# Kernel tuning notes

Measured on AMD Instinct MI355X. Metric: run time of the kernel, lower is better.

The kernel has to match this reference:

```python
import jax, jax.numpy as jnp
import numpy as np

EPS = 1e-10
TOP_K = 2  # experts_per_token


def setup_inputs() -> dict:
    key = jax.random.key(0)
    k1, k2 = jax.random.split(key)
    dim, E = 2048, 64
    B, S = 4, 4096
    x = jax.random.normal(k1, (B * S, dim), dtype=jnp.float32)
    W = jax.random.normal(k2, (dim, E), dtype=jnp.float32) * (1.0 / np.sqrt(dim))
    b = jnp.zeros((E,), dtype=jnp.float32)
    return {"x": x, "W": W, "b": b, "batch_size": B, "seq_len": S}


def reference(x, W, b, batch_size, seq_len):
    E = W.shape[1]
    N = x.shape[0]  # batch_size * seq_len
    # gate + softmax + clamp
    scores = jax.nn.softmax(x @ W + b, axis=1)
    scores = jnp.clip(scores, EPS, 1.0 - EPS)
    # log-odds transform and rz loss over (seq, experts) per batch
    logits = jnp.log(scores / (1.0 - scores)).reshape(batch_size, seq_len, E)
    rz_loss = jnp.mean(jax.scipy.special.logsumexp(logits, axis=(1, 2)))
    # top-k experts per token
    top_scores, sel_idx = jax.lax.top_k(scores, TOP_K)  # (N, K) each
    flat_idx = sel_idx.reshape(-1)  # (N*K,)
    # histogram of assignments per expert (torch.histc with unit bins)
    num_tokens_per_expert = jax.ops.segment_sum(
        jnp.ones_like(flat_idx, dtype=jnp.float32), flat_idx, num_segments=E)
    # stable argsort groups slots by expert id, preserving token order
    perm = jnp.argsort(flat_idx, stable=True)  # (N*K,)
    top_scores_sorted = top_scores.reshape(-1)[perm]
    token_indices_experts_sorted = perm // TOP_K
    return (top_scores_sorted, token_indices_experts_sorted,
            num_tokens_per_expert, rz_loss)
```

## Files before the change

kernel.cpp:

```cpp
#include <hip/hip_runtime.h>
#include <math.h>

#define EPS_ 1e-10f
#define MARGIN 4e-3f

typedef __attribute__((ext_vector_type(8))) short sh8;
typedef __attribute__((ext_vector_type(4))) float fx4;

__device__ __forceinline__ bool betterf(float v, int i, float w, int j) {
    return (v > w) || (v == w && i < j);
}
__device__ __forceinline__ bool betterd(double v, int i, double w, int j) {
    return (v > w) || (v == w && i < j);
}
__device__ __forceinline__ unsigned short f2bf(float f) {
    unsigned u = __float_as_uint(f);
    u += 0x7fffu + ((u >> 16) & 1u);
    return (unsigned short)(u >> 16);
}
__device__ __forceinline__ float bf2f(unsigned short h) {
    return __uint_as_float(((unsigned)h) << 16);
}
__device__ __forceinline__ void cvt8(const float4 a, const float4 c, sh8& hi, sh8& lo) {
    const float v[8] = {a.x, a.y, a.z, a.w, c.x, c.y, c.z, c.w};
#pragma unroll
    for (int j = 0; j < 8; ++j) {
        const unsigned short h = f2bf(v[j]);
        hi[j] = (short)h;
        lo[j] = (short)f2bf(v[j] - bf2f(h));
    }
}

__global__ __launch_bounds__(256)
void wconv(const float* __restrict__ W, unsigned short* __restrict__ wf)
{
    const int gid = blockIdx.x * 256 + threadIdx.x;
    const int e = gid & 63, k = gid >> 6;
    const int s = k >> 5, kk = k & 31, bq = kk >> 3, j = kk & 7;
    const int t = e >> 4, n = e & 15;
    const int l = n + 16 * bq;
    const float w = W[(size_t)k * 64 + e];
    const unsigned short hi = f2bf(w);
    const unsigned short lo = f2bf(w - bf2f(hi));
    const size_t base = ((size_t)s * 4 + t) * 2;
    wf[(base + 0) * 512 + l * 8 + j] = hi;
    wf[(base + 1) * 512 + l * 8 + j] = lo;
}

#define NKS 4
__global__ __launch_bounds__(256, 4)
void gemm_mfma(const float* __restrict__ x, const unsigned short* __restrict__ wfg,
               const float* __restrict__ b, int dim, int N,
               float* __restrict__ ts, int* __restrict__ sel,
               float* __restrict__ rzrow,
               int* __restrict__ nflags, int* __restrict__ flaglist)
{
    __shared__ float red[3][64][17];

    const int tid  = threadIdx.x;
    const int lane = tid & 63;
    const int wv   = tid >> 6;
    const int r0   = blockIdx.x * 16;
    const int kslice = dim / NKS;
    const int k0   = wv * kslice;
    const int nstep = kslice / 32;

    const int m = lane & 15;
    const int q = lane >> 4;

    fx4 acc[4] = {};

    const float* xp = x + (size_t)(r0 + m) * dim + k0 + q * 8;
    const unsigned short* wbase = wfg + ((size_t)(k0 / 32) * 4096) + lane * 8;

    float4 xa = *(const float4*)xp;
    float4 xb = *(const float4*)(xp + 4);

    for (int w = 0; w < nstep; ++w) {
        sh8 ahi, alo;
        cvt8(xa, xb, ahi, alo);

        if (w + 1 < nstep) {
            xa = *(const float4*)(xp + (size_t)(w + 1) * 32);
            xb = *(const float4*)(xp + (size_t)(w + 1) * 32 + 4);
        }

        const unsigned short* wk = wbase + (size_t)w * 4096;
        sh8 bhi[4], blo[4];
#pragma unroll
        for (int t = 0; t < 4; ++t) {
            bhi[t] = __builtin_bit_cast(sh8, *(const int4*)(wk + (t * 2 + 0) * 512));
            blo[t] = __builtin_bit_cast(sh8, *(const int4*)(wk + (t * 2 + 1) * 512));
        }
#pragma unroll
        for (int t = 0; t < 4; ++t)
            acc[t] = __builtin_amdgcn_mfma_f32_16x16x32_bf16(ahi, bhi[t], acc[t], 0, 0, 0);
#pragma unroll
        for (int t = 0; t < 4; ++t)
            acc[t] = __builtin_amdgcn_mfma_f32_16x16x32_bf16(ahi, blo[t], acc[t], 0, 0, 0);
#pragma unroll
        for (int t = 0; t < 4; ++t)
            acc[t] = __builtin_amdgcn_mfma_f32_16x16x32_bf16(alo, bhi[t], acc[t], 0, 0, 0);
    }

    if (wv > 0) {
#pragma unroll
        for (int t = 0; t < 4; ++t)
#pragma unroll
            for (int i = 0; i < 4; ++i)
                red[wv - 1][lane][t * 4 + i] = acc[t][i];
    }
    __syncthreads();
    if (wv != 0) return;

#pragma unroll
    for (int s = 0; s < 3; ++s)
#pragma unroll
        for (int t = 0; t < 4; ++t)
#pragma unroll
            for (int i = 0; i < 4; ++i)
                acc[t][i] += red[s][lane][t * 4 + i];

    const int n = lane & 15;
    const int g = lane >> 4;
    float bb[4];
#pragma unroll
    for (int t = 0; t < 4; ++t) bb[t] = b[t * 16 + n];

#pragma unroll
    for (int i = 0; i < 4; ++i) {
        const int row = r0 + g * 4 + i;
        float z[4];
#pragma unroll
        for (int t = 0; t < 4; ++t) z[t] = acc[t][i] + bb[t];

        float v1 = -3.4e38f, v2 = -3.4e38f;
        int i1 = 1 << 30, i2 = 1 << 30;
#pragma unroll
        for (int t = 0; t < 4; ++t) {
            const float v = z[t];
            const int e = t * 16 + n;
            if (v > v1)      { v2 = v1; i2 = i1; v1 = v; i1 = e; }
            else if (v > v2) { v2 = v;  i2 = e; }
        }
#pragma unroll
        for (int mm = 1; mm < 16; mm <<= 1) {
            const float w1 = __shfl_xor(v1, mm, 16); const int j1 = __shfl_xor(i1, mm, 16);
            const float w2 = __shfl_xor(v2, mm, 16); const int j2 = __shfl_xor(i2, mm, 16);
            if (betterf(w1, j1, v1, i1)) {
                float nv2; int ni2;
                if (betterf(v1, i1, w2, j2)) { nv2 = v1; ni2 = i1; }
                else                         { nv2 = w2; ni2 = j2; }
                v1 = w1; i1 = j1; v2 = nv2; i2 = ni2;
            } else if (betterf(w1, j1, v2, i2)) { v2 = w1; i2 = j1; }
        }

        float m3 = -3.4e38f;
#pragma unroll
        for (int t = 0; t < 4; ++t) {
            const int e = t * 16 + n;
            const bool skip = (e == i1) || (e == i2);
            m3 = skip ? m3 : fmaxf(m3, z[t]);
        }
#pragma unroll
        for (int mm = 1; mm < 16; mm <<= 1) m3 = fmaxf(m3, __shfl_xor(m3, mm, 16));

        float sloc[4], ssum = 0.0f;
#pragma unroll
        for (int t = 0; t < 4; ++t) { sloc[t] = expf(z[t] - v1); ssum += sloc[t]; }
#pragma unroll
        for (int mm = 1; mm < 16; mm <<= 1) ssum += __shfl_xor(ssum, mm, 16);
        const float inv = 1.0f / ssum;
        float srz = 0.0f;
#pragma unroll
        for (int t = 0; t < 4; ++t) {
            float sc = fminf(fmaxf(sloc[t] * inv, EPS_), 1.0f - EPS_);
            srz += sc / (1.0f - sc);
        }
#pragma unroll
        for (int mm = 1; mm < 16; mm <<= 1) srz += __shfl_xor(srz, mm, 16);

        if (n == 0) {
            const float s1 = fminf(fmaxf(inv, EPS_), 1.0f - EPS_);
            const float s2 = fminf(fmaxf(expf(v2 - v1) * inv, EPS_), 1.0f - EPS_);
            ts[row * 2 + 0] = s1;
            ts[row * 2 + 1] = s2;
            sel[row * 2 + 0] = i1;
            sel[row * 2 + 1] = i2;
            rzrow[row] = srz;
            if ((v1 - v2) < MARGIN || (v2 - m3) < MARGIN) {
                const int slot = atomicAdd(nflags, 1);
                flaglist[slot] = row;
            }
        }
    }
}

__global__ __launch_bounds__(1024)
void fixup(const float* __restrict__ x, const float* __restrict__ W,
           const float* __restrict__ b, int dim,
           const int* __restrict__ nflags, const int* __restrict__ flaglist,
           float* __restrict__ ts, int* __restrict__ sel)
{
    __shared__ double red[1024];
    const int tid = threadIdx.x;
    const int e = tid & 63;
    const int q = tid >> 6;
    const int nf = *nflags;
    const int slice = dim >> 4;

    for (int f = blockIdx.x; f < nf; f += gridDim.x) {
        const int row = flaglist[f];
        const float* xr = x + (size_t)row * dim;
        const int k0 = q * slice;
        double a0 = 0.0, a1 = 0.0, a2 = 0.0, a3 = 0.0;
        for (int k = k0; k < k0 + slice; k += 4) {
            a0 = fma((double)xr[k + 0], (double)W[(size_t)(k + 0) * 64 + e], a0);
            a1 = fma((double)xr[k + 1], (double)W[(size_t)(k + 1) * 64 + e], a1);
            a2 = fma((double)xr[k + 2], (double)W[(size_t)(k + 2) * 64 + e], a2);
            a3 = fma((double)xr[k + 3], (double)W[(size_t)(k + 3) * 64 + e], a3);
        }
        red[tid] = (a0 + a1) + (a2 + a3);
        __syncthreads();
        for (int st = 512; st >= 64; st >>= 1) {
            if (tid < st) red[tid] += red[tid + st];
            __syncthreads();
        }
        if (tid < 64) {
            const double z = red[tid] + (double)b[e];
            double v1 = z, v2 = -1e300;
            int i1 = e, i2 = 1 << 30;
#pragma unroll
            for (int mm = 1; mm < 64; mm <<= 1) {
                const double w1 = __shfl_xor(v1, mm, 64); const int j1 = __shfl_xor(i1, mm, 64);
                const double w2 = __shfl_xor(v2, mm, 64); const int j2 = __shfl_xor(i2, mm, 64);
                if (betterd(w1, j1, v1, i1)) {
                    double nv2; int ni2;
                    if (betterd(v1, i1, w2, j2)) { nv2 = v1; ni2 = i1; }
                    else                         { nv2 = w2; ni2 = j2; }
                    v1 = w1; i1 = j1; v2 = nv2; i2 = ni2;
                } else if (betterd(w1, j1, v2, i2)) { v2 = w1; i2 = j1; }
            }
            float sl = expf((float)(z - v1));
            float ssum = sl;
#pragma unroll
            for (int mm = 1; mm < 64; mm <<= 1) ssum += __shfl_xor(ssum, mm, 64);
            const float inv = 1.0f / ssum;
            if (e == 0) {
                const float s1 = fminf(fmaxf(inv, EPS_), 1.0f - EPS_);
                const float s2 = fminf(fmaxf(expf((float)(v2 - v1)) * inv, EPS_), 1.0f - EPS_);
                ts[row * 2 + 0] = s1;
                ts[row * 2 + 1] = s2;
                sel[row * 2 + 0] = i1;
                sel[row * 2 + 1] = i2;
            }
        }
        __syncthreads();
    }
}

__global__ void hist_chunks(const int* __restrict__ sel, int nchunks,
                            int* __restrict__ hist, int* __restrict__ cnt2)
{
    __shared__ int cnt[64];
    const int lane = threadIdx.x;
    const int c = blockIdx.x;
    cnt[lane] = 0;
    __syncthreads();
    const int ex = sel[c * 64 + lane];
    atomicAdd(&cnt[ex], 1);
    __syncthreads();
    cnt2[(size_t)lane * nchunks + c] = cnt[lane];
    if (cnt[lane]) atomicAdd(&hist[lane], cnt[lane]);
}

__global__ void rz_batch(const float* __restrict__ rzrow,
                         const int* __restrict__ bs_p, const int* __restrict__ sl_p,
                         double* __restrict__ bsum)
{
    __shared__ double red[256];
    const int nb = bs_p[0];
    const int seq = sl_p[0];
    for (int bb = blockIdx.x; bb < nb; bb += gridDim.x) {
        double s = 0.0;
        for (int i = threadIdx.x; i < seq; i += 256)
            s += (double)rzrow[(size_t)bb * seq + i];
        red[threadIdx.x] = s;
        __syncthreads();
        for (int st = 128; st > 0; st >>= 1) {
            if (threadIdx.x < st) red[threadIdx.x] += red[threadIdx.x + st];
            __syncthreads();
        }
        if (threadIdx.x == 0) bsum[bb] = red[0];
        __syncthreads();
    }
}

__global__ void combine(const int* __restrict__ hist,
                        int* __restrict__ estart,
                        const double* __restrict__ bsum,
                        const int* __restrict__ bs_p,
                        float* __restrict__ out_cnt, float* __restrict__ out_rz)
{
    const int e = threadIdx.x;
    const int c0 = hist[e];
    int incl = c0;
#pragma unroll
    for (int mm = 1; mm < 64; mm <<= 1) {
        const int w = __shfl_up(incl, mm, 64);
        if (e >= mm) incl += w;
    }
    estart[e] = incl - c0;
    out_cnt[e] = (float)c0;
    if (e == 0) {
        const int nb = bs_p[0];
        double a = 0.0;
        for (int i = 0; i < nb; ++i) a += log(bsum[i]);
        out_rz[0] = (float)(a / nb);
    }
}

__global__ __launch_bounds__(1024)
void chunk_scan(const int* __restrict__ cnt2, const int* __restrict__ estart,
                int nchunks, int* __restrict__ cbase)
{
    __shared__ int sc[1024];
    const int e = blockIdx.x;
    const int t = threadIdx.x;
    const int v = (t < nchunks) ? cnt2[(size_t)e * nchunks + t] : 0;
    sc[t] = v;
    __syncthreads();
#pragma unroll
    for (int off = 1; off < 1024; off <<= 1) {
        const int add = (t >= off) ? sc[t - off] : 0;
        __syncthreads();
        sc[t] += add;
        __syncthreads();
    }
    if (t < nchunks)
        cbase[(size_t)t * 64 + e] = estart[e] + sc[t] - v;
}

__global__ void scatter(const int* __restrict__ sel, const float* __restrict__ ts,
                        const int* __restrict__ cbase,
                        float* __restrict__ out_sc, float* __restrict__ out_idx)
{
    __shared__ int shx[64];
    const int lane = threadIdx.x;
    const int c = blockIdx.x;
    const int idx = c * 64 + lane;
    const int ex = sel[idx];
    shx[lane] = ex;
    __syncthreads();
    int pre = 0;
#pragma unroll
    for (int j = 0; j < 64; ++j) pre += (int)((j < lane) && (shx[j] == ex));
    const int pos = cbase[c * 64 + ex] + pre;
    out_sc[pos]  = ts[idx];
    out_idx[pos] = (float)(idx >> 1);
}

extern "C" void kernel_launch(void* const* d_in, const int* in_sizes, int n_in,
                              void* d_out, int out_size, void* d_ws, size_t ws_size,
                              hipStream_t stream)
{
    const float* x = (const float*)d_in[0];
    const float* W = (const float*)d_in[1];
    const float* b = (const float*)d_in[2];
    const int* bs_p = (const int*)d_in[3];
    const int* sl_p = (const int*)d_in[4];

    const int E   = in_sizes[2];
    const int dim = in_sizes[1] / E;
    const int N   = in_sizes[0] / dim;
    const int total = N * 2;
    const int nchunks = total / 64;

    char* ws = (char*)d_ws;
    size_t off = 0;
    int*    hist     = (int*)(ws + off); off += 256;
    double* bsum     = (double*)(ws + off); off += 512;
    int*    nflags   = (int*)(ws + off); off += 256;
    int*    estart   = (int*)(ws + off); off += 256;
    float*  ts       = (float*)(ws + off); off += (size_t)total * 4;
    int*    sel      = (int*)(ws + off); off += (size_t)total * 4;
    int*    flaglist = (int*)(ws + off); off += (size_t)N * 4;
    float*  rzrow    = (float*)(ws + off); off += (size_t)N * 4;
    int*    cnt2     = (int*)(ws + off); off += (size_t)nchunks * 64 * 4;
    int*    cbase    = (int*)(ws + off); off += (size_t)nchunks * 64 * 4;
    unsigned short* wfg = (unsigned short*)(ws + off); off += (size_t)dim * 64 * 2 * 2;

    float* out_sc  = (float*)d_out;
    float* out_idx = out_sc + total;
    float* out_cnt = out_idx + total;
    float* out_rz  = out_cnt + E;

    hipMemsetAsync(ws, 0, 1280, stream);

    hipLaunchKernelGGL(wconv, dim3(dim * 64 / 256), dim3(256), 0, stream, W, wfg);
    hipLaunchKernelGGL(gemm_mfma, dim3(N / 16), dim3(256), 0, stream,
                       x, wfg, b, dim, N, ts, sel, rzrow, nflags, flaglist);
    hipLaunchKernelGGL(fixup, dim3(512), dim3(1024), 0, stream,
                       x, W, b, dim, nflags, flaglist, ts, sel);
    hipLaunchKernelGGL(hist_chunks, dim3(nchunks), dim3(64), 0, stream,
                       sel, nchunks, hist, cnt2);
    hipLaunchKernelGGL(rz_batch, dim3(64), dim3(256), 0, stream,
                       rzrow, bs_p, sl_p, bsum);
    hipLaunchKernelGGL(combine, dim3(1), dim3(64), 0, stream,
                       hist, estart, bsum, bs_p, out_cnt, out_rz);
    hipLaunchKernelGGL(chunk_scan, dim3(64), dim3(1024), 0, stream,
                       cnt2, estart, nchunks, cbase);
    hipLaunchKernelGGL(scatter, dim3(nchunks), dim3(64), 0, stream,
                       sel, ts, cbase, out_sc, out_idx);
}
```

Before: 102.4 us.

## Tile gate GEMM over 64 rows with 8 k-split waves and tree reduction

The gate GEMM block now handles 64 rows instead of 16 and splits K across 8 waves instead of 4. Each B fragment loaded from global memory is reused across four row tiles, with double-buffered weight loads. Partial sums are combined through a shared-memory tree reduction, and the softmax/top-2 epilogue is spread across all waves, one expert per lane. This cuts redundant weight traffic and per-row overhead, at the cost of far more accumulator registers (64 floats per lane), a larger shared-memory footprint, and more barriers.

```diff
diff --git a/kernel.cpp b/kernel.cpp
--- a/kernel.cpp
+++ b/kernel.cpp
@@ -47,140 +47,219 @@
     wf[(base + 1) * 512 + l * 8 + j] = lo;
 }
 
-#define NKS 4
-__global__ __launch_bounds__(256, 4)
+__global__ __launch_bounds__(512, 2)
 void gemm_mfma(const float* __restrict__ x, const unsigned short* __restrict__ wfg,
                const float* __restrict__ b, int dim, int N,
                float* __restrict__ ts, int* __restrict__ sel,
                float* __restrict__ rzrow,
                int* __restrict__ nflags, int* __restrict__ flaglist)
 {
-    __shared__ float red[3][64][17];
+    __shared__ float slots[4][64][65];
 
     const int tid  = threadIdx.x;
     const int lane = tid & 63;
     const int wv   = tid >> 6;
-    const int r0   = blockIdx.x * 16;
-    const int kslice = dim / NKS;
+    const int r0   = blockIdx.x * 64;
+    const int kslice = dim >> 3;
     const int k0   = wv * kslice;
-    const int nstep = kslice / 32;
+    const int nstep = kslice >> 5;
 
     const int m = lane & 15;
     const int q = lane >> 4;
 
-    fx4 acc[4] = {};
-
-    const float* xp = x + (size_t)(r0 + m) * dim + k0 + q * 8;
-    const unsigned short* wbase = wfg + ((size_t)(k0 / 32) * 4096) + lane * 8;
-
-    float4 xa = *(const float4*)xp;
-    float4 xb = *(const float4*)(xp + 4);
-
-    for (int w = 0; w < nstep; ++w) {
-        sh8 ahi, alo;
-        cvt8(xa, xb, ahi, alo);
-
-        if (w + 1 < nstep) {
-            xa = *(const float4*)(xp + (size_t)(w + 1) * 32);
-            xb = *(const float4*)(xp + (size_t)(w + 1) * 32 + 4);
-        }
-
-        const unsigned short* wk = wbase + (size_t)w * 4096;
-        sh8 bhi[4], blo[4];
-#pragma unroll
-        for (int t = 0; t < 4; ++t) {
-            bhi[t] = __builtin_bit_cast(sh8, *(const int4*)(wk + (t * 2 + 0) * 512));
-            blo[t] = __builtin_bit_cast(sh8, *(const int4*)(wk + (t * 2 + 1) * 512));
-        }
+    fx4 acc[4][4];
+#pragma unroll
+    for (int t = 0; t < 4; ++t)
+#pragma unroll
+        for (int te = 0; te < 4; ++te)
+            acc[t][te] = (fx4){0.f, 0.f, 0.f, 0.f};
+
+    const float* xp0 = x + (size_t)(r0 +  0 + m) * dim + k0 + q * 8;
+    const float* xp1 = x + (size_t)(r0 + 16 + m) * dim + k0 + q * 8;
+    const float* xp2 = x + (size_t)(r0 + 32 + m) * dim + k0 + q * 8;
+    const float* xp3 = x + (size_t)(r0 + 48 + m) * dim + k0 + q * 8;
+    const unsigned short* wbase = wfg + (size_t)(k0 >> 5) * 4096 + lane * 8;
+
+    sh8 w0h[4], w0l[4], w1h[4], w1l[4];
+#pragma unroll
+    for (int te = 0; te < 4; ++te) {
+        w0h[te] = __builtin_bit_cast(sh8, *(const int4*)(wbase + (te * 2 + 0) * 512));
+        w0l[te] = __builtin_bit_cast(sh8, *(const int4*)(wbase + (te * 2 + 1) * 512));
+    }
+
+    for (int w = 0; w < nstep; w += 2) {
+        {
+            const unsigned short* wk = wbase + (size_t)(w + 1) * 4096;
+#pragma unroll
+            for (int te = 0; te < 4; ++te) {
+                w1h[te] = __builtin_bit_cast(sh8, *(const int4*)(wk + (te * 2 + 0) * 512));
+                w1l[te] = __builtin_bit_cast(sh8, *(const int4*)(wk + (te * 2 + 1) * 512));
+            }
+        }
+        {
+            float4 xa0 = *(const float4*)(xp0 + (size_t)w * 32);
+            float4 xb0 = *(const float4*)(xp0 + (size_t)w * 32 + 4);
+            float4 xa1 = *(const float4*)(xp1 + (size_t)w * 32);
+            float4 xb1 = *(const float4*)(xp1 + (size_t)w * 32 + 4);
+            float4 xa2 = *(const float4*)(xp2 + (size_t)w * 32);
+            float4 xb2 = *(const float4*)(xp2 + (size_t)w * 32 + 4);
+            float4 xa3 = *(const float4*)(xp3 + (size_t)w * 32);
+            float4 xb3 = *(const float4*)(xp3 + (size_t)w * 32 + 4);
+            sh8 ah, al;
+            cvt8(xa0, xb0, ah, al);
+#pragma unroll
+            for (int te = 0; te < 4; ++te) {
+                acc[0][te] = __builtin_amdgcn_mfma_f32_16x16x32_bf16(ah, w0h[te], acc[0][te], 0, 0, 0);
+                acc[0][te] = __builtin_amdgcn_mfma_f32_16x16x32_bf16(ah, w0l[te], acc[0][te], 0, 0, 0);
+                acc[0][te] = __builtin_amdgcn_mfma_f32_16x16x32_bf16(al, w0h[te], acc[0][te], 0, 0, 0);
+            }
+            cvt8(xa1, xb1, ah, al);
+#pragma unroll
+            for (int te = 0; te < 4; ++te) {
+                acc[1][te] = __builtin_amdgcn_mfma_f32_16x16x32_bf16(ah, w0h[te], acc[1][te], 0, 0, 0);
+                acc[1][te] = __builtin_amdgcn_mfma_f32_16x16x32_bf16(ah, w0l[te], acc[1][te], 0, 0, 0);
+                acc[1][te] = __builtin_amdgcn_mfma_f32_16x16x32_bf16(al, w0h[te], acc[1][te], 0, 0, 0);
+            }
+            cvt8(xa2, xb2, ah, al);
+#pragma unroll
+            for (int te = 0; te < 4; ++te) {
+                acc[2][te] = __builtin_amdgcn_mfma_f32_16x16x32_bf16(ah, w0h[te], acc[2][te], 0, 0, 0);
+                acc[2][te] = __builtin_amdgcn_mfma_f32_16x16x32_bf16(ah, w0l[te], acc[2][te], 0, 0, 0);
+                acc[2][te] = __builtin_amdgcn_mfma_f32_16x16x32_bf16(al, w0h[te], acc[2][te], 0, 0, 0);
+            }
+            cvt8(xa3, xb3, ah, al);
+#pragma unroll
+            for (int te = 0; te < 4; ++te) {
+                acc[3][te] = __builtin_amdgcn_mfma_f32_16x16x32_bf16(ah, w0h[te], acc[3][te], 0, 0, 0);
+                acc[3][te] = __builtin_amdgcn_mfma_f32_16x16x32_bf16(ah, w0l[te], acc[3][te], 0, 0, 0);
+                acc[3][te] = __builtin_amdgcn_mfma_f32_16x16x32_bf16(al, w0h[te], acc[3][te], 0, 0, 0);
+            }
+        }
+        if (w + 2 < nstep) {
+            const unsigned short* wk = wbase + (size_t)(w + 2) * 4096;
+#pragma unroll
+            for (int te = 0; te < 4; ++te) {
+                w0h[te] = __builtin_bit_cast(sh8, *(const int4*)(wk + (te * 2 + 0) * 512));
+                w0l[te] = __builtin_bit_cast(sh8, *(const int4*)(wk + (te * 2 + 1) * 512));
+            }
+        }
+        {
+            const int w1 = w + 1;
+            float4 xa0 = *(const float4*)(xp0 + (size_t)w1 * 32);
+            float4 xb0 = *(const float4*)(xp0 + (size_t)w1 * 32 + 4);
+            float4 xa1 = *(const float4*)(xp1 + (size_t)w1 * 32);
+            float4 xb1 = *(const float4*)(xp1 + (size_t)w1 * 32 + 4);
+            float4 xa2 = *(const float4*)(xp2 + (size_t)w1 * 32);
+            float4 xb2 = *(const float4*)(xp2 + (size_t)w1 * 32 + 4);
+            float4 xa3 = *(const float4*)(xp3 + (size_t)w1 * 32);
+            float4 xb3 = *(const float4*)(xp3 + (size_t)w1 * 32 + 4);
+            sh8 ah, al;
+            cvt8(xa0, xb0, ah, al);
+#pragma unroll
+            for (int te = 0; te < 4; ++te) {
+                acc[0][te] = __builtin_amdgcn_mfma_f32_16x16x32_bf16(ah, w1h[te], acc[0][te], 0, 0, 0);
+                acc[0][te] = __builtin_amdgcn_mfma_f32_16x16x32_bf16(ah, w1l[te], acc[0][te], 0, 0, 0);
+                acc[0][te] = __builtin_amdgcn_mfma_f32_16x16x32_bf16(al, w1h[te], acc[0][te], 0, 0, 0);
+            }
+            cvt8(xa1, xb1, ah, al);
+#pragma unroll
+            for (int te = 0; te < 4; ++te) {
+                acc[1][te] = __builtin_amdgcn_mfma_f32_16x16x32_bf16(ah, w1h[te], acc[1][te], 0, 0, 0);
+                acc[1][te] = __builtin_amdgcn_mfma_f32_16x16x32_bf16(ah, w1l[te], acc[1][te], 0, 0, 0);
+                acc[1][te] = __builtin_amdgcn_mfma_f32_16x16x32_bf16(al, w1h[te], acc[1][te], 0, 0, 0);
+            }
+            cvt8(xa2, xb2, ah, al);
+#pragma unroll
+            for (int te = 0; te < 4; ++te) {
+                acc[2][te] = __builtin_amdgcn_mfma_f32_16x16x32_bf16(ah, w1h[te], acc[2][te], 0, 0, 0);
+                acc[2][te] = __builtin_amdgcn_mfma_f32_16x16x32_bf16(ah, w1l[te], acc[2][te], 0, 0, 0);
+                acc[2][te] = __builtin_amdgcn_mfma_f32_16x16x32_bf16(al, w1h[te], acc[2][te], 0, 0, 0);
+            }
+            cvt8(xa3, xb3, ah, al);
+#pragma unroll
+            for (int te = 0; te < 4; ++te) {
+                acc[3][te] = __builtin_amdgcn_mfma_f32_16x16x32_bf16(ah, w1h[te], acc[3][te], 0, 0, 0);
+                acc[3][te] = __builtin_amdgcn_mfma_f32_16x16x32_bf16(ah, w1l[te], acc[3][te], 0, 0, 0);
+                acc[3][te] = __builtin_amdgcn_mfma_f32_16x16x32_bf16(al, w1h[te], acc[3][te], 0, 0, 0);
+            }
+        }
+    }
+
+    const int n = lane & 15;
+#pragma unroll
+    for (int s = 4; s >= 1; s >>= 1) {
+        if (wv >= s && wv < 2 * s) {
+            float (*slot)[65] = slots[wv - s];
+#pragma unroll
+            for (int t = 0; t < 4; ++t)
+#pragma unroll
+                for (int te = 0; te < 4; ++te)
+#pragma unroll
+                    for (int i = 0; i < 4; ++i)
+                        slot[t * 16 + q * 4 + i][te * 16 + n] = acc[t][te][i];
+        }
+        __syncthreads();
+        if (wv < s) {
+            float (*slot)[65] = slots[wv];
+#pragma unroll
+            for (int t = 0; t < 4; ++t)
+#pragma unroll
+                for (int te = 0; te < 4; ++te)
+#pragma unroll
+                    for (int i = 0; i < 4; ++i)
+                        acc[t][te][i] += slot[t * 16 + q * 4 + i][te * 16 + n];
+        }
+        __syncthreads();
+    }
+
+    if (wv == 0) {
 #pragma unroll
         for (int t = 0; t < 4; ++t)
-            acc[t] = __builtin_amdgcn_mfma_f32_16x16x32_bf16(ahi, bhi[t], acc[t], 0, 0, 0);
-#pragma unroll
-        for (int t = 0; t < 4; ++t)
-            acc[t] = __builtin_amdgcn_mfma_f32_16x16x32_bf16(ahi, blo[t], acc[t], 0, 0, 0);
-#pragma unroll
-        for (int t = 0; t < 4; ++t)
-            acc[t] = __builtin_amdgcn_mfma_f32_16x16x32_bf16(alo, bhi[t], acc[t], 0, 0, 0);
-    }
-
-    if (wv > 0) {
-#pragma unroll
-        for (int t = 0; t < 4; ++t)
-#pragma unroll
-            for (int i = 0; i < 4; ++i)
-                red[wv - 1][lane][t * 4 + i] = acc[t][i];
+#pragma unroll
+            for (int te = 0; te < 4; ++te)
+#pragma unroll
+                for (int i = 0; i < 4; ++i)
+                    slots[0][t * 16 + q * 4 + i][te * 16 + n] = acc[t][te][i];
     }
     __syncthreads();
-    if (wv != 0) return;
-
-#pragma unroll
-    for (int s = 0; s < 3; ++s)
-#pragma unroll
-        for (int t = 0; t < 4; ++t)
-#pragma unroll
-            for (int i = 0; i < 4; ++i)
-                acc[t][i] += red[s][lane][t * 4 + i];
-
-    const int n = lane & 15;
-    const int g = lane >> 4;
-    float bb[4];
-#pragma unroll
-    for (int t = 0; t < 4; ++t) bb[t] = b[t * 16 + n];
-
-#pragma unroll
-    for (int i = 0; i < 4; ++i) {
-        const int row = r0 + g * 4 + i;
-        float z[4];
-#pragma unroll
-        for (int t = 0; t < 4; ++t) z[t] = acc[t][i] + bb[t];
-
-        float v1 = -3.4e38f, v2 = -3.4e38f;
-        int i1 = 1 << 30, i2 = 1 << 30;
-#pragma unroll
-        for (int t = 0; t < 4; ++t) {
-            const float v = z[t];
-            const int e = t * 16 + n;
-            if (v > v1)      { v2 = v1; i2 = i1; v1 = v; i1 = e; }
-            else if (v > v2) { v2 = v;  i2 = e; }
-        }
-#pragma unroll
-        for (int mm = 1; mm < 16; mm <<= 1) {
-            const float w1 = __shfl_xor(v1, mm, 16); const int j1 = __shfl_xor(i1, mm, 16);
-            const float w2 = __shfl_xor(v2, mm, 16); const int j2 = __shfl_xor(i2, mm, 16);
-            if (betterf(w1, j1, v1, i1)) {
+
+    const int e = lane;
+    const float be = b[e];
+    for (int rr = 0; rr < 8; ++rr) {
+        const int lrow = wv * 8 + rr;
+        const int row = r0 + lrow;
+        const float z = slots[0][lrow][e] + be;
+
+        float v1 = z, v2 = -3.4e38f;
+        int i1 = e, i2 = 1 << 30;
+#pragma unroll
+        for (int mm = 1; mm < 64; mm <<= 1) {
+            const float wva = __shfl_xor(v1, mm, 64); const int j1 = __shfl_xor(i1, mm, 64);
+            const float wvb = __shfl_xor(v2, mm, 64); const int j2 = __shfl_xor(i2, mm, 64);
+            if (betterf(wva, j1, v1, i1)) {
                 float nv2; int ni2;
-                if (betterf(v1, i1, w2, j2)) { nv2 = v1; ni2 = i1; }
-                else                         { nv2 = w2; ni2 = j2; }
-                v1 = w1; i1 = j1; v2 = nv2; i2 = ni2;
-            } else if (betterf(w1, j1, v2, i2)) { v2 = w1; i2 = j1; }
-        }
-
-        float m3 = -3.4e38f;
-#pragma unroll
-        for (int t = 0; t < 4; ++t) {
-            const int e = t * 16 + n;
-            const bool skip = (e == i1) || (e == i2);
-            m3 = skip ? m3 : fmaxf(m3, z[t]);
-        }
-#pragma unroll
-        for (int mm = 1; mm < 16; mm <<= 1) m3 = fmaxf(m3, __shfl_xor(m3, mm, 16));
-
-        float sloc[4], ssum = 0.0f;
-#pragma unroll
-        for (int t = 0; t < 4; ++t) { sloc[t] = expf(z[t] - v1); ssum += sloc[t]; }
-#pragma unroll
-        for (int mm = 1; mm < 16; mm <<= 1) ssum += __shfl_xor(ssum, mm, 16);
+                if (betterf(v1, i1, wvb, j2)) { nv2 = v1; ni2 = i1; }
+                else                          { nv2 = wvb; ni2 = j2; }
+                v1 = wva; i1 = j1; v2 = nv2; i2 = ni2;
+            } else if (betterf(wva, j1, v2, i2)) { v2 = wva; i2 = j1; }
+        }
+
+        float m3 = (e == i1 || e == i2) ? -3.4e38f : z;
+#pragma unroll
+        for (int mm = 1; mm < 64; mm <<= 1) m3 = fmaxf(m3, __shfl_xor(m3, mm, 64));
+
+        const float ex = expf(z - v1);
+        float ssum = ex;
+#pragma unroll
+        for (int mm = 1; mm < 64; mm <<= 1) ssum += __shfl_xor(ssum, mm, 64);
         const float inv = 1.0f / ssum;
-        float srz = 0.0f;
-#pragma unroll
-        for (int t = 0; t < 4; ++t) {
-            float sc = fminf(fmaxf(sloc[t] * inv, EPS_), 1.0f - EPS_);
-            srz += sc / (1.0f - sc);
-        }
-#pragma unroll
-        for (int mm = 1; mm < 16; mm <<= 1) srz += __shfl_xor(srz, mm, 16);
-
-        if (n == 0) {
+
+        float sc = fminf(fmaxf(ex * inv, EPS_), 1.0f - EPS_);
+        float srz = sc / (1.0f - sc);
+#pragma unroll
+        for (int mm = 1; mm < 64; mm <<= 1) srz += __shfl_xor(srz, mm, 64);
+
+        if (e == 0) {
             const float s1 = fminf(fmaxf(inv, EPS_), 1.0f - EPS_);
             const float s2 = fminf(fmaxf(expf(v2 - v1) * inv, EPS_), 1.0f - EPS_);
             ts[row * 2 + 0] = s1;
@@ -189,8 +268,8 @@
             sel[row * 2 + 1] = i2;
             rzrow[row] = srz;
             if ((v1 - v2) < MARGIN || (v2 - m3) < MARGIN) {
-                const int slot = atomicAdd(nflags, 1);
-                flaglist[slot] = row;
+                const int slot2 = atomicAdd(nflags, 1);
+                flaglist[slot2] = row;
             }
         }
     }
@@ -398,7 +477,7 @@
     hipMemsetAsync(ws, 0, 1280, stream);
 
     hipLaunchKernelGGL(wconv, dim3(dim * 64 / 256), dim3(256), 0, stream, W, wfg);
-    hipLaunchKernelGGL(gemm_mfma, dim3(N / 16), dim3(256), 0, stream,
+    hipLaunchKernelGGL(gemm_mfma, dim3(N / 64), dim3(512), 0, stream,
                        x, wfg, b, dim, N, ts, sel, rzrow, nflags, flaglist);
     hipLaunchKernelGGL(fixup, dim3(512), dim3(1024), 0, stream,
                        x, W, b, dim, nflags, flaglist, ts, sel);
```

Measured after the change: 99.66 us. 2.7% less time.

## Give each wave full-K ownership of 16 rows with LDS-staged x and register double-buffered W

Applied to the files above, without the earlier changes.

The gate GEMM now gives each block 64 rows, and each wave owns 16 of them across the full K range. Before, four waves split K and then reduced their partial sums through shared memory. The x tile is converted to bf16 hi/lo pairs and written into a swizzled, double-buffered LDS window of 128 columns, and W fragments are prefetched into alternating register sets. The epilogue moves from 16-lane groups to full 64-lane shuffles, with one expert per lane. The aim is to remove the cross-wave reduction and improve load pipelining, at the cost of dropping to one block per CU with large LDS use and fewer resident waves to hide latency.

```diff
diff --git a/kernel.cpp b/kernel.cpp
--- a/kernel.cpp
+++ b/kernel.cpp
@@ -21,14 +21,12 @@
 __device__ __forceinline__ float bf2f(unsigned short h) {
     return __uint_as_float(((unsigned)h) << 16);
 }
-__device__ __forceinline__ void cvt8(const float4 a, const float4 c, sh8& hi, sh8& lo) {
-    const float v[8] = {a.x, a.y, a.z, a.w, c.x, c.y, c.z, c.w};
-#pragma unroll
-    for (int j = 0; j < 8; ++j) {
-        const unsigned short h = f2bf(v[j]);
-        hi[j] = (short)h;
-        lo[j] = (short)f2bf(v[j] - bf2f(h));
-    }
+__device__ __forceinline__ void cvt4(const float4 v, uint2& hp, uint2& lp) {
+    const unsigned short h0 = f2bf(v.x), h1 = f2bf(v.y), h2 = f2bf(v.z), h3 = f2bf(v.w);
+    const unsigned short l0 = f2bf(v.x - bf2f(h0)), l1 = f2bf(v.y - bf2f(h1));
+    const unsigned short l2 = f2bf(v.z - bf2f(h2)), l3 = f2bf(v.w - bf2f(h3));
+    hp.x = h0 | ((unsigned)h1 << 16); hp.y = h2 | ((unsigned)h3 << 16);
+    lp.x = l0 | ((unsigned)l1 << 16); lp.y = l2 | ((unsigned)l3 << 16);
 }
 
 __global__ __launch_bounds__(256)
@@ -47,140 +45,157 @@
     wf[(base + 1) * 512 + l * 8 + j] = lo;
 }
 
-#define NKS 4
-__global__ __launch_bounds__(256, 4)
+#define KWIN 128
+__global__ __launch_bounds__(256, 1)
 void gemm_mfma(const float* __restrict__ x, const unsigned short* __restrict__ wfg,
                const float* __restrict__ b, int dim, int N,
                float* __restrict__ ts, int* __restrict__ sel,
                float* __restrict__ rzrow,
                int* __restrict__ nflags, int* __restrict__ flaglist)
 {
-    __shared__ float red[3][64][17];
+    __shared__ __align__(16) char smem[82176];
 
     const int tid  = threadIdx.x;
     const int lane = tid & 63;
     const int wv   = tid >> 6;
-    const int r0   = blockIdx.x * 16;
-    const int kslice = dim / NKS;
-    const int k0   = wv * kslice;
-    const int nstep = kslice / 32;
-
-    const int m = lane & 15;
-    const int q = lane >> 4;
+    const int r0   = blockIdx.x * 64;
+    const int nwin = dim / KWIN;
+    const int nks  = dim >> 5;
+
+    const int m   = lane & 15;
+    const int q   = lane >> 4;
+    const int l31 = lane & 31;
+    const int l5  = lane >> 5;
+    const int lh  = l31 & 1;
+    const int lc  = l31 >> 1;
 
     fx4 acc[4] = {};
 
-    const float* xp = x + (size_t)(r0 + m) * dim + k0 + q * 8;
-    const unsigned short* wbase = wfg + ((size_t)(k0 / 32) * 4096) + lane * 8;
-
-    float4 xa = *(const float4*)xp;
-    float4 xb = *(const float4*)(xp + 4);
-
-    for (int w = 0; w < nstep; ++w) {
-        sh8 ahi, alo;
-        cvt8(xa, xb, ahi, alo);
-
-        if (w + 1 < nstep) {
-            xa = *(const float4*)(xp + (size_t)(w + 1) * 32);
-            xb = *(const float4*)(xp + (size_t)(w + 1) * 32 + 4);
-        }
-
-        const unsigned short* wk = wbase + (size_t)w * 4096;
-        sh8 bhi[4], blo[4];
-#pragma unroll
-        for (int t = 0; t < 4; ++t) {
-            bhi[t] = __builtin_bit_cast(sh8, *(const int4*)(wk + (t * 2 + 0) * 512));
-            blo[t] = __builtin_bit_cast(sh8, *(const int4*)(wk + (t * 2 + 1) * 512));
-        }
-#pragma unroll
-        for (int t = 0; t < 4; ++t)
-            acc[t] = __builtin_amdgcn_mfma_f32_16x16x32_bf16(ahi, bhi[t], acc[t], 0, 0, 0);
-#pragma unroll
-        for (int t = 0; t < 4; ++t)
-            acc[t] = __builtin_amdgcn_mfma_f32_16x16x32_bf16(ahi, blo[t], acc[t], 0, 0, 0);
-#pragma unroll
-        for (int t = 0; t < 4; ++t)
-            acc[t] = __builtin_amdgcn_mfma_f32_16x16x32_bf16(alo, bhi[t], acc[t], 0, 0, 0);
-    }
-
-    if (wv > 0) {
-#pragma unroll
-        for (int t = 0; t < 4; ++t)
-#pragma unroll
-            for (int i = 0; i < 4; ++i)
-                red[wv - 1][lane][t * 4 + i] = acc[t][i];
-    }
+    char* const base = smem;
+    const unsigned short* wl8 = wfg + lane * 8;
+
+    sh8 wAh[4], wAl[4], wBh[4], wBl[4];
+#pragma unroll
+    for (int te = 0; te < 4; ++te) {
+        wAh[te] = __builtin_bit_cast(sh8, *(const int4*)(wl8 + (te * 2 + 0) * 512));
+        wAl[te] = __builtin_bit_cast(sh8, *(const int4*)(wl8 + (te * 2 + 1) * 512));
+    }
+
+    float4 xa[8];
+#pragma unroll
+    for (int i = 0; i < 8; ++i) {
+        const int row = wv * 16 + i * 2 + l5;
+        xa[i] = *(const float4*)(x + (size_t)(r0 + row) * dim + l31 * 4);
+    }
+#pragma unroll
+    for (int i = 0; i < 8; ++i) {
+        const int row = wv * 16 + i * 2 + l5;
+        const int sc = lc ^ (row & 15);
+        uint2 hp, lp; cvt4(xa[i], hp, lp);
+        *(uint2*)(base + row * 256 + sc * 16 + lh * 8) = hp;
+        *(uint2*)(base + 16384 + row * 256 + sc * 16 + lh * 8) = lp;
+    }
+
+    const int arow = wv * 16 + m;
+
+#define WSTEP(S, CH, CL, PH, PL)                                                    \
+    {                                                                               \
+        const int ks = w * 4 + S;                                                   \
+        if (ks + 1 < nks) {                                                         \
+            const unsigned short* wk = wl8 + (size_t)(ks + 1) * 4096;               \
+            _Pragma("unroll")                                                       \
+            for (int te = 0; te < 4; ++te) {                                        \
+                PH[te] = __builtin_bit_cast(sh8, *(const int4*)(wk + (te * 2 + 0) * 512)); \
+                PL[te] = __builtin_bit_cast(sh8, *(const int4*)(wk + (te * 2 + 1) * 512)); \
+            }                                                                       \
+        }                                                                           \
+        const int sc = (S * 4 + q) ^ m;                                             \
+        const sh8 ah = __builtin_bit_cast(sh8,                                      \
+            *(const int4*)(base + cb * 32768 + arow * 256 + sc * 16));              \
+        const sh8 al = __builtin_bit_cast(sh8,                                      \
+            *(const int4*)(base + cb * 32768 + 16384 + arow * 256 + sc * 16));      \
+        _Pragma("unroll")                                                           \
+        for (int te = 0; te < 4; ++te) {                                            \
+            acc[te] = __builtin_amdgcn_mfma_f32_16x16x32_bf16(ah, CH[te], acc[te], 0, 0, 0); \
+            acc[te] = __builtin_amdgcn_mfma_f32_16x16x32_bf16(ah, CL[te], acc[te], 0, 0, 0); \
+            acc[te] = __builtin_amdgcn_mfma_f32_16x16x32_bf16(al, CH[te], acc[te], 0, 0, 0); \
+        }                                                                           \
+    }
+
+    for (int w = 0; w < nwin; ++w) {
+        const int cb = w & 1;
+        const int tb = cb ^ 1;
+        const bool more = (w + 1 < nwin);
+        if (more) {
+#pragma unroll
+            for (int i = 0; i < 8; ++i) {
+                const int row = wv * 16 + i * 2 + l5;
+                xa[i] = *(const float4*)(x + (size_t)(r0 + row) * dim
+                                           + (size_t)(w + 1) * KWIN + l31 * 4);
+            }
+        }
+        WSTEP(0, wAh, wAl, wBh, wBl)
+        WSTEP(1, wBh, wBl, wAh, wAl)
+        WSTEP(2, wAh, wAl, wBh, wBl)
+        WSTEP(3, wBh, wBl, wAh, wAl)
+        if (more) {
+#pragma unroll
+            for (int i = 0; i < 8; ++i) {
+                const int row = wv * 16 + i * 2 + l5;
+                const int sc = lc ^ (row & 15);
+                uint2 hp, lp; cvt4(xa[i], hp, lp);
+                *(uint2*)(base + tb * 32768 + row * 256 + sc * 16 + lh * 8) = hp;
+                *(uint2*)(base + tb * 32768 + 16384 + row * 256 + sc * 16 + lh * 8) = lp;
+            }
+        }
+    }
+#undef WSTEP
+
+    float* slots = (float*)(base + 65536);
+#pragma unroll
+    for (int te = 0; te < 4; ++te)
+#pragma unroll
+        for (int i = 0; i < 4; ++i)
+            slots[(wv * 16 + q * 4 + i) * 65 + te * 16 + m] = acc[te][i];
     __syncthreads();
-    if (wv != 0) return;
-
-#pragma unroll
-    for (int s = 0; s < 3; ++s)
-#pragma unroll
-        for (int t = 0; t < 4; ++t)
-#pragma unroll
-            for (int i = 0; i < 4; ++i)
-                acc[t][i] += red[s][lane][t * 4 + i];
-
-    const int n = lane & 15;
-    const int g = lane >> 4;
-    float bb[4];
-#pragma unroll
-    for (int t = 0; t < 4; ++t) bb[t] = b[t * 16 + n];
-
-#pragma unroll
-    for (int i = 0; i < 4; ++i) {
-        const int row = r0 + g * 4 + i;
-        float z[4];
-#pragma unroll
-        for (int t = 0; t < 4; ++t) z[t] = acc[t][i] + bb[t];
-
-        float v1 = -3.4e38f, v2 = -3.4e38f;
-        int i1 = 1 << 30, i2 = 1 << 30;
-#pragma unroll
-        for (int t = 0; t < 4; ++t) {
-            const float v = z[t];
-            const int e = t * 16 + n;
-            if (v > v1)      { v2 = v1; i2 = i1; v1 = v; i1 = e; }
-            else if (v > v2) { v2 = v;  i2 = e; }
-        }
-#pragma unroll
-        for (int mm = 1; mm < 16; mm <<= 1) {
-            const float w1 = __shfl_xor(v1, mm, 16); const int j1 = __shfl_xor(i1, mm, 16);
-            const float w2 = __shfl_xor(v2, mm, 16); const int j2 = __shfl_xor(i2, mm, 16);
-            if (betterf(w1, j1, v1, i1)) {
+
+    const int e = lane;
+    const float be = b[e];
+    for (int rr = 0; rr < 16; ++rr) {
+        const int lrow = wv * 16 + rr;
+        const int row = r0 + lrow;
+        const float z = slots[lrow * 65 + e] + be;
+
+        float v1 = z, v2 = -3.4e38f;
+        int i1 = e, i2 = 1 << 30;
+#pragma unroll
+        for (int mm = 1; mm < 64; mm <<= 1) {
+            const float wva = __shfl_xor(v1, mm, 64); const int j1 = __shfl_xor(i1, mm, 64);
+            const float wvb = __shfl_xor(v2, mm, 64); const int j2 = __shfl_xor(i2, mm, 64);
+            if (betterf(wva, j1, v1, i1)) {
                 float nv2; int ni2;
-                if (betterf(v1, i1, w2, j2)) { nv2 = v1; ni2 = i1; }
-                else                         { nv2 = w2; ni2 = j2; }
-                v1 = w1; i1 = j1; v2 = nv2; i2 = ni2;
-            } else if (betterf(w1, j1, v2, i2)) { v2 = w1; i2 = j1; }
-        }
-
-        float m3 = -3.4e38f;
-#pragma unroll
-        for (int t = 0; t < 4; ++t) {
-            const int e = t * 16 + n;
-            const bool skip = (e == i1) || (e == i2);
-            m3 = skip ? m3 : fmaxf(m3, z[t]);
-        }
-#pragma unroll
-        for (int mm = 1; mm < 16; mm <<= 1) m3 = fmaxf(m3, __shfl_xor(m3, mm, 16));
-
-        float sloc[4], ssum = 0.0f;
-#pragma unroll
-        for (int t = 0; t < 4; ++t) { sloc[t] = expf(z[t] - v1); ssum += sloc[t]; }
-#pragma unroll
-        for (int mm = 1; mm < 16; mm <<= 1) ssum += __shfl_xor(ssum, mm, 16);
+                if (betterf(v1, i1, wvb, j2)) { nv2 = v1; ni2 = i1; }
+                else                          { nv2 = wvb; ni2 = j2; }
+                v1 = wva; i1 = j1; v2 = nv2; i2 = ni2;
+            } else if (betterf(wva, j1, v2, i2)) { v2 = wva; i2 = j1; }
+        }
+
+        float m3 = (e == i1 || e == i2) ? -3.4e38f : z;
+#pragma unroll
+        for (int mm = 1; mm < 64; mm <<= 1) m3 = fmaxf(m3, __shfl_xor(m3, mm, 64));
+
+        const float ex = expf(z - v1);
+        float ssum = ex;
+#pragma unroll
+        for (int mm = 1; mm < 64; mm <<= 1) ssum += __shfl_xor(ssum, mm, 64);
         const float inv = 1.0f / ssum;
-        float srz = 0.0f;
-#pragma unroll
-        for (int t = 0; t < 4; ++t) {
-            float sc = fminf(fmaxf(sloc[t] * inv, EPS_), 1.0f - EPS_);
-            srz += sc / (1.0f - sc);
-        }
-#pragma unroll
-        for (int mm = 1; mm < 16; mm <<= 1) srz += __shfl_xor(srz, mm, 16);
-
-        if (n == 0) {
+
+        float sc2 = fminf(fmaxf(ex * inv, EPS_), 1.0f - EPS_);
+        float srz = sc2 / (1.0f - sc2);
+#pragma unroll
+        for (int mm = 1; mm < 64; mm <<= 1) srz += __shfl_xor(srz, mm, 64);
+
+        if (e == 0) {
             const float s1 = fminf(fmaxf(inv, EPS_), 1.0f - EPS_);
             const float s2 = fminf(fmaxf(expf(v2 - v1) * inv, EPS_), 1.0f - EPS_);
             ts[row * 2 + 0] = s1;
@@ -189,8 +204,8 @@
             sel[row * 2 + 1] = i2;
             rzrow[row] = srz;
             if ((v1 - v2) < MARGIN || (v2 - m3) < MARGIN) {
-                const int slot = atomicAdd(nflags, 1);
-                flaglist[slot] = row;
+                const int slot2 = atomicAdd(nflags, 1);
+                flaglist[slot2] = row;
             }
         }
     }
@@ -398,7 +413,7 @@
     hipMemsetAsync(ws, 0, 1280, stream);
 
     hipLaunchKernelGGL(wconv, dim3(dim * 64 / 256), dim3(256), 0, stream, W, wfg);
-    hipLaunchKernelGGL(gemm_mfma, dim3(N / 16), dim3(256), 0, stream,
+    hipLaunchKernelGGL(gemm_mfma, dim3(N / 64), dim3(256), 0, stream,
                        x, wfg, b, dim, N, ts, sel, rzrow, nflags, flaglist);
     hipLaunchKernelGGL(fixup, dim3(512), dim3(1024), 0, stream,
                        x, W, b, dim, nflags, flaglist, ts, sel);
```

Result: slower. 124.0 us (+21.1%).
